# Performance work log

Hardware: AMD Instinct MI355X
Metric: run time of the kernel (lower is better)

The kernel has to match this reference:

```python
import jax, jax.numpy as jnp
import numpy as np

EPS = 1e-5

def _leaky(x):
    return jax.nn.leaky_relu(x, 0.2)

def _bn(x, p, axis):
    # p: [4, C] rows = (gamma, beta, running_mean, running_var); inference-mode BN
    g, b, m, v = p
    scale = g * jax.lax.rsqrt(v + EPS)
    shape = [1] * x.ndim
    shape[axis] = -1
    return x * scale.reshape(shape) + (b - m * scale).reshape(shape)

def _graph_feature(x, k):
    # x: [B, C, N] -> edge features [B, 2C, N, k] (knn on -squared-distance, topk largest)
    B, C, N = x.shape
    xx = jnp.sum(x * x, axis=1)                                   # [B, N]
    pd = 2.0 * jnp.einsum('bcn,bcm->bnm', x, x) - xx[:, :, None] - xx[:, None, :]
    idx = jax.lax.top_k(pd, k)[1]                                 # [B, N, k]
    xt = jnp.transpose(x, (0, 2, 1))                              # [B, N, C]
    nb = xt[jnp.arange(B)[:, None, None], idx]                    # [B, N, k, C]
    ctr = xt[:, :, None, :]
    f = jnp.concatenate([nb - ctr, jnp.broadcast_to(ctr, nb.shape)], axis=-1)
    return jnp.transpose(f, (0, 3, 1, 2))                         # [B, 2C, N, k]

def _cbam(x, fc1, fc2, sw):
    # Channel attention (shared MLP on avg+max pooled) then spatial attention (5x5 conv)
    mlp = lambda v: jax.nn.relu(v @ fc1.T) @ fc2.T
    ca = jax.nn.sigmoid(mlp(jnp.mean(x, (2, 3))) + mlp(jnp.max(x, (2, 3))))
    x = x * ca[:, :, None, None]
    s = jnp.concatenate([jnp.mean(x, 1, keepdims=True), jnp.max(x, 1, keepdims=True)], axis=1)
    sa = jax.lax.conv_general_dilated(s, sw, (1, 1), [(2, 2), (2, 2)],
                                      dimension_numbers=('NCHW', 'OIHW', 'NCHW'))
    return x * jax.nn.sigmoid(sa)

def _edge_block(x, k, W, bn, fc1, fc2, sw):
    f = _graph_feature(x, k)                                      # [B, 2C, N, k]
    f = _leaky(_bn(jnp.einsum('oc,bcnk->bonk', W, f), bn, 1))     # 1x1 conv + BN + LeakyReLU
    f = _cbam(f, fc1, fc2, sw)
    return jnp.max(f, axis=-1)                                    # [B, Cout, N]

def _bn_params(key, c):
    k1, k2, k3, k4 = jax.random.split(key, 4)
    g = 1.0 + 0.1 * jax.random.normal(k1, (c,))
    b = 0.1 * jax.random.normal(k2, (c,))
    m = 0.1 * jax.random.normal(k3, (c,))
    v = 0.5 + jax.random.uniform(k4, (c,))
    return jnp.stack([g, b, m, v])

def setup_inputs() -> dict:
    key = jax.random.key(0)
    nrm = lambda i, shape, s: s * jax.random.normal(jax.random.fold_in(key, i), shape, dtype=jnp.float32)
    d = {}
    d['x'] = jax.random.normal(jax.random.fold_in(key, 0), (4, 3, 2048), dtype=jnp.float32)
    d['W1'] = nrm(1, (64, 6), 0.3)
    d['W2'] = nrm(2, (64, 128), 0.15)
    d['W3'] = nrm(3, (128, 128), 0.15)
    d['W4'] = nrm(4, (256, 256), 0.1)
    d['W5'] = nrm(5, (1024, 512), 0.08)
    for i, c in zip(range(1, 6), [64, 64, 128, 256, 1024]):
        d['bn%d' % i] = _bn_params(jax.random.fold_in(key, 10 + i), c)
    d['bn6'] = _bn_params(jax.random.fold_in(key, 16), 512)
    d['bn7'] = _bn_params(jax.random.fold_in(key, 17), 256)
    for j, c in zip(range(1, 5), [64, 64, 128, 256]):
        r = c // 8
        d['ca%d_fc1' % j] = nrm(20 + j, (r, c), 0.2)
        d['ca%d_fc2' % j] = nrm(30 + j, (c, r), 0.2)
        d['sa%d' % j] = nrm(40 + j, (1, 2, 5, 5), 0.2)
    d['lin1_w'] = nrm(50, (512, 2048), 0.05)
    d['lin2_w'] = nrm(51, (256, 512), 0.08)
    d['lin2_b'] = nrm(52, (256,), 0.05)
    d['lin3_w'] = nrm(53, (40, 256), 0.1)
    d['lin3_b'] = nrm(54, (40,), 0.05)
    d['k'] = 20
    return d

def reference(x, W1, bn1, ca1_fc1, ca1_fc2, sa1, W2, bn2, ca2_fc1, ca2_fc2, sa2,
              W3, bn3, ca3_fc1, ca3_fc2, sa3, W4, bn4, ca4_fc1, ca4_fc2, sa4,
              W5, bn5, lin1_w, bn6, lin2_w, lin2_b, bn7, lin3_w, lin3_b, k):
    x1 = _edge_block(x,  k, W1, bn1, ca1_fc1, ca1_fc2, sa1)   # [B, 64, N]
    x2 = _edge_block(x1, k, W2, bn2, ca2_fc1, ca2_fc2, sa2)   # [B, 64, N]
    x3 = _edge_block(x2, k, W3, bn3, ca3_fc1, ca3_fc2, sa3)   # [B, 128, N]
    x4 = _edge_block(x3, k, W4, bn4, ca4_fc1, ca4_fc2, sa4)   # [B, 256, N]
    xc = jnp.concatenate([x1, x2, x3, x4], axis=1)            # [B, 512, N]
    h = _leaky(_bn(jnp.einsum('oc,bcn->bon', W5, xc), bn5, 1))  # [B, 1024, N]
    g = jnp.concatenate([jnp.max(h, axis=-1), jnp.mean(h, axis=-1)], axis=1)  # [B, 2048]
    g = _leaky(_bn(g @ lin1_w.T, bn6, 1))                     # dropout = identity (eval)
    g = _leaky(_bn(g @ lin2_w.T + lin2_b, bn7, 1))
    return g @ lin3_w.T + lin3_b                              # [B, 40]
```

## Files before the change

kernel.cpp:

```cpp
#include <hip/hip_runtime.h>
#include <math.h>

#define BB 4
#define NN 2048
#define KK 20
#define EPSF 1e-5f
#define TR 4

__device__ __forceinline__ float leaky(float x){ return x > 0.f ? x : 0.2f*x; }
__device__ __forceinline__ float sigm(float x){ return 1.f/(1.f+expf(-x)); }

__device__ __forceinline__ unsigned wave_umax_dpp(unsigned x){
  unsigned t;
  t = (unsigned)__builtin_amdgcn_update_dpp(0, (int)x, 0x111, 0xf, 0xf, true); x = x > t ? x : t;
  t = (unsigned)__builtin_amdgcn_update_dpp(0, (int)x, 0x112, 0xf, 0xf, true); x = x > t ? x : t;
  t = (unsigned)__builtin_amdgcn_update_dpp(0, (int)x, 0x114, 0xf, 0xf, true); x = x > t ? x : t;
  t = (unsigned)__builtin_amdgcn_update_dpp(0, (int)x, 0x118, 0xf, 0xf, true); x = x > t ? x : t;
  t = (unsigned)__builtin_amdgcn_update_dpp(0, (int)x, 0x142, 0xf, 0xf, true); x = x > t ? x : t;
  t = (unsigned)__builtin_amdgcn_update_dpp(0, (int)x, 0x143, 0xf, 0xf, true); x = x > t ? x : t;
  return (unsigned)__builtin_amdgcn_readlane((int)x, 63);
}

__global__ void k_xx(const float* __restrict__ X, long bstride, int C, float* __restrict__ xx){
  int i = blockIdx.x*blockDim.x + threadIdx.x;
  int b = i >> 11, n = i & (NN-1);
  const float* xb = X + (long)b*bstride;
  float s = 0.f;
  for (int c = 0; c < C; ++c){ float v = xb[c*NN + n]; s += v*v; }
  xx[i] = s;
}

__global__ __launch_bounds__(256) void k_knn(const float* __restrict__ X, long bstride, int C,
                      const float* __restrict__ xx, int* __restrict__ idx){
  __shared__ unsigned int pdrow[TR][NN];
  int rowsPerB = NN/TR;
  int b = blockIdx.x / rowsPerB;
  int r0 = (blockIdx.x % rowsPerB) * TR;
  const float* xb = X + (long)b*bstride;
  const float* xxb = xx + b*NN;
  int tid = threadIdx.x;
  int m0 = tid << 3;

  float acc[4][8];
  #pragma unroll
  for (int r = 0; r < 4; ++r)
    #pragma unroll
    for (int j = 0; j < 8; ++j) acc[r][j] = 0.f;
  for (int c = 0; c < C; ++c){
    const float* xcp = xb + (long)c*NN;
    float4 ctr = *(const float4*)(xcp + r0);
    float4 va = *(const float4*)(xcp + m0);
    float4 vb = *(const float4*)(xcp + m0 + 4);
    float v[8] = {va.x,va.y,va.z,va.w,vb.x,vb.y,vb.z,vb.w};
    #pragma unroll
    for (int j = 0; j < 8; ++j){
      acc[0][j] = fmaf(ctr.x, v[j], acc[0][j]);
      acc[1][j] = fmaf(ctr.y, v[j], acc[1][j]);
      acc[2][j] = fmaf(ctr.z, v[j], acc[2][j]);
      acc[3][j] = fmaf(ctr.w, v[j], acc[3][j]);
    }
  }
  float4 xr4 = *(const float4*)(xxb + r0);
  float xxr[4] = {xr4.x, xr4.y, xr4.z, xr4.w};
  float4 xma = *(const float4*)(xxb + m0);
  float4 xmb = *(const float4*)(xxb + m0 + 4);
  float xm[8] = {xma.x,xma.y,xma.z,xma.w,xmb.x,xmb.y,xmb.z,xmb.w};
  #pragma unroll
  for (int r = 0; r < 4; ++r){
    unsigned u[8];
    #pragma unroll
    for (int j = 0; j < 8; ++j){
      float pd = 2.f*acc[r][j] - xxr[r] - xm[j];
      unsigned uu = __float_as_uint(pd);
      uu ^= (uu & 0x80000000u) ? 0xFFFFFFFFu : 0x80000000u;
      u[j] = uu;
    }
    *(uint4*)&pdrow[r][m0]     = make_uint4(u[0],u[1],u[2],u[3]);
    *(uint4*)&pdrow[r][m0 + 4] = make_uint4(u[4],u[5],u[6],u[7]);
  }
  __syncthreads();

  int wave = tid >> 6, lane = tid & 63;
  int r = wave;
  unsigned long long k1 = 0ull, k2 = 0ull;
  #pragma unroll
  for (int j = 0; j < 32; ++j){
    int m = lane + (j<<6);
    unsigned long long key = ((unsigned long long)pdrow[r][m] << 11) | (unsigned)(2047 - m);
    if (key > k1){ k2 = k1; k1 = key; }
    else if (key > k2){ k2 = key; }
  }
  unsigned removed = 0u;
  int* orow = idx + ((long)b*NN + r0 + r)*KK;
  for (int sel = 0; sel < KK; ++sel){
    unsigned p = (unsigned)(k1 >> 11);
    unsigned g = wave_umax_dpp(p);
    unsigned long long tied = __ballot(p == g);
    if (__builtin_popcountll(tied) > 1){
      unsigned low = (p == g) ? (unsigned)(k1 & 2047ull) : 0u;
      unsigned gl = wave_umax_dpp(low);
      tied = __ballot((p == g) && (low == gl));
    }
    int owner = (int)__builtin_ctzll(tied);
    if (lane == owner){
      int gm = 2047 - (int)(k1 & 2047ull);
      orow[sel] = gm;
      removed |= 1u << (gm >> 6);
      k1 = k2; k2 = 0ull;
      if (k1 == 0ull && sel < KK-1){
        #pragma unroll
        for (int j = 0; j < 32; ++j){
          if (removed & (1u << j)) continue;
          int m = lane + (j<<6);
          unsigned long long key = ((unsigned long long)pdrow[r][m] << 11) | (unsigned)(2047 - m);
          if (key > k1){ k2 = k1; k1 = key; }
          else if (key > k2){ k2 = key; }
        }
      }
    }
  }
}

__global__ void k_proj(const float* __restrict__ X, long bstride, int C, int Cout,
                       const float* __restrict__ W, const float* __restrict__ bn,
                       float* __restrict__ Pg, float* __restrict__ PgT,
                       float* __restrict__ Pc, float* __restrict__ PcT){
  int nb = NN/256;
  int t = blockIdx.x;
  int nchunk = t % nb; t /= nb;
  int o = t % Cout; int b = t / Cout;
  int m = nchunk*256 + threadIdx.x;
  const float* xb = X + (long)b*bstride;
  float a1 = 0.f, a2 = 0.f;
  for (int c = 0; c < C; ++c){
    float v  = xb[c*NN + m];
    float wl = W[o*2*C + c], wr = W[o*2*C + C + c];
    a1 += wl*v; a2 += (wr - wl)*v;
  }
  float gg = bn[o], bb = bn[Cout+o], mn = bn[2*Cout+o], vv = bn[3*Cout+o];
  float scale = gg * rsqrtf(vv + EPSF);
  float bias  = bb - mn*scale;
  float pg = scale*a1;
  float pc = scale*a2 + bias;
  Pg [((long)b*Cout + o)*NN + m] = pg;
  PgT[((long)b*NN + m)*Cout + o] = pg;
  Pc [((long)b*Cout + o)*NN + m] = pc;
  PcT[((long)b*NN + m)*Cout + o] = pc;
}

__global__ __launch_bounds__(256) void k_proj_t(const float* __restrict__ X, long bstride, int C, int Cout,
                         const float* __restrict__ W, const float* __restrict__ bn,
                         float* __restrict__ Pg, float* __restrict__ PgT,
                         float* __restrict__ Pc, float* __restrict__ PcT){
  __shared__ float xs[32][128];
  __shared__ float wls[64][33];
  __shared__ float wds[64][33];
  int t = blockIdx.x;
  int nb = t & 15; t >>= 4;
  int nob = Cout >> 6;
  int ob = t % nob; int b = t / nob;
  int n0 = nb << 7, o0 = ob << 6;
  int tid = threadIdx.x;
  int tx = tid & 15, ty = tid >> 4;
  const float* xb = X + (long)b*bstride + n0;

  float ag[4][8], ac[4][8];
  #pragma unroll
  for (int i = 0; i < 4; ++i)
    #pragma unroll
    for (int j = 0; j < 8; ++j){ ag[i][j] = 0.f; ac[i][j] = 0.f; }

  for (int cc = 0; cc < C; cc += 32){
    {
      int col4 = tid & 31;
      int ci0 = tid >> 5;
      #pragma unroll
      for (int q = 0; q < 4; ++q){
        int ci = ci0 + (q << 3);
        float4 v = *(const float4*)(xb + (long)(cc + ci)*NN + (col4 << 2));
        *(float4*)&xs[ci][col4 << 2] = v;
      }
    }
    {
      int ci4 = tid & 7;
      int oi0 = tid >> 3;
      #pragma unroll
      for (int q = 0; q < 2; ++q){
        int oi = oi0 + (q << 5);
        const float* wrow = W + (long)(o0 + oi)*2*C + cc + (ci4 << 2);
        float4 wl = *(const float4*)(wrow);
        float4 wr = *(const float4*)(wrow + C);
        wls[oi][(ci4 << 2) + 0] = wl.x;
        wls[oi][(ci4 << 2) + 1] = wl.y;
        wls[oi][(ci4 << 2) + 2] = wl.z;
        wls[oi][(ci4 << 2) + 3] = wl.w;
        wds[oi][(ci4 << 2) + 0] = wr.x - wl.x;
        wds[oi][(ci4 << 2) + 1] = wr.y - wl.y;
        wds[oi][(ci4 << 2) + 2] = wr.z - wl.z;
        wds[oi][(ci4 << 2) + 3] = wr.w - wl.w;
      }
    }
    __syncthreads();
    #pragma unroll 8
    for (int ci = 0; ci < 32; ++ci){
      float4 xa  = *(const float4*)&xs[ci][tx << 2];
      float4 xc2 = *(const float4*)&xs[ci][64 + (tx << 2)];
      #pragma unroll
      for (int oo = 0; oo < 4; ++oo){
        float wl = wls[(ty << 2) + oo][ci];
        float wd = wds[(ty << 2) + oo][ci];
        ag[oo][0] = fmaf(wl, xa.x, ag[oo][0]); ag[oo][1] = fmaf(wl, xa.y, ag[oo][1]);
        ag[oo][2] = fmaf(wl, xa.z, ag[oo][2]); ag[oo][3] = fmaf(wl, xa.w, ag[oo][3]);
        ag[oo][4] = fmaf(wl, xc2.x, ag[oo][4]); ag[oo][5] = fmaf(wl, xc2.y, ag[oo][5]);
        ag[oo][6] = fmaf(wl, xc2.z, ag[oo][6]); ag[oo][7] = fmaf(wl, xc2.w, ag[oo][7]);
        ac[oo][0] = fmaf(wd, xa.x, ac[oo][0]); ac[oo][1] = fmaf(wd, xa.y, ac[oo][1]);
        ac[oo][2] = fmaf(wd, xa.z, ac[oo][2]); ac[oo][3] = fmaf(wd, xa.w, ac[oo][3]);
        ac[oo][4] = fmaf(wd, xc2.x, ac[oo][4]); ac[oo][5] = fmaf(wd, xc2.y, ac[oo][5]);
        ac[oo][6] = fmaf(wd, xc2.z, ac[oo][6]); ac[oo][7] = fmaf(wd, xc2.w, ac[oo][7]);
      }
    }
    __syncthreads();
  }

  float scl[4], bia[4];
  #pragma unroll
  for (int oo = 0; oo < 4; ++oo){
    int o = o0 + (ty << 2) + oo;
    scl[oo] = bn[o] * rsqrtf(bn[3*Cout + o] + EPSF);
    bia[oo] = bn[Cout + o] - bn[2*Cout + o]*scl[oo];
  }
  #pragma unroll
  for (int oo = 0; oo < 4; ++oo){
    long rb = ((long)b*Cout + o0 + (ty << 2) + oo)*NN + n0;
    float4 g0 = {scl[oo]*ag[oo][0], scl[oo]*ag[oo][1], scl[oo]*ag[oo][2], scl[oo]*ag[oo][3]};
    float4 g1 = {scl[oo]*ag[oo][4], scl[oo]*ag[oo][5], scl[oo]*ag[oo][6], scl[oo]*ag[oo][7]};
    float4 c0 = {fmaf(scl[oo], ac[oo][0], bia[oo]), fmaf(scl[oo], ac[oo][1], bia[oo]),
                 fmaf(scl[oo], ac[oo][2], bia[oo]), fmaf(scl[oo], ac[oo][3], bia[oo])};
    float4 c1 = {fmaf(scl[oo], ac[oo][4], bia[oo]), fmaf(scl[oo], ac[oo][5], bia[oo]),
                 fmaf(scl[oo], ac[oo][6], bia[oo]), fmaf(scl[oo], ac[oo][7], bia[oo])};
    *(float4*)(Pg + rb + (tx << 2))      = g0;
    *(float4*)(Pg + rb + 64 + (tx << 2)) = g1;
    *(float4*)(Pc + rb + (tx << 2))      = c0;
    *(float4*)(Pc + rb + 64 + (tx << 2)) = c1;
  }
  #pragma unroll
  for (int j = 0; j < 8; ++j){
    int n = n0 + ((j < 4) ? (tx << 2) + j : 64 + (tx << 2) + (j - 4));
    long rb = ((long)b*NN + n)*Cout + o0 + (ty << 2);
    float4 tg = {scl[0]*ag[0][j], scl[1]*ag[1][j], scl[2]*ag[2][j], scl[3]*ag[3][j]};
    float4 tc = {fmaf(scl[0], ac[0][j], bia[0]), fmaf(scl[1], ac[1][j], bia[1]),
                 fmaf(scl[2], ac[2][j], bia[2]), fmaf(scl[3], ac[3][j], bia[3])};
    *(float4*)(PgT + rb) = tg;
    *(float4*)(PcT + rb) = tc;
  }
}

__global__ void k_cstats(const float* __restrict__ Pg, const float* __restrict__ Pc,
                         const int* __restrict__ idx, int Cout,
                         float* __restrict__ cmean, float* __restrict__ cmax){
  int b = blockIdx.x / Cout, o = blockIdx.x % Cout;
  const float* pg = Pg + ((long)b*Cout + o)*NN;
  const float* pc = Pc + ((long)b*Cout + o)*NN;
  const int* id = idx + (long)b*NN*KK;
  int tid = threadIdx.x;
  float s = 0.f, mx = -INFINITY;
  for (int i = tid; i < NN*KK; i += 256){
    int n = i / KK;
    int iv = id[i];
    float v = leaky(pg[iv] + pc[n]);
    s += v; mx = fmaxf(mx, v);
  }
  __shared__ float ss[256], sm[256];
  ss[tid] = s; sm[tid] = mx; __syncthreads();
  for (int st = 128; st; st >>= 1){
    if (tid < st){ ss[tid] += ss[tid+st]; sm[tid] = fmaxf(sm[tid], sm[tid+st]); }
    __syncthreads();
  }
  if (tid == 0){ cmean[blockIdx.x] = ss[0]/(float)(NN*KK); cmax[blockIdx.x] = sm[0]; }
}

__global__ void k_catt(const float* __restrict__ cmean, const float* __restrict__ cmax,
                       const float* __restrict__ fc1, const float* __restrict__ fc2,
                       int Cout, int r, float* __restrict__ ca){
  int b = blockIdx.x, tid = threadIdx.x;
  __shared__ float h1m[32], h1x[32];
  __shared__ float mv[256], xv[256];
  if (tid < Cout){ mv[tid] = cmean[b*Cout+tid]; xv[tid] = cmax[b*Cout+tid]; }
  __syncthreads();
  if (tid < r){
    float am = 0.f, ax = 0.f;
    for (int c = 0; c < Cout; ++c){ float w = fc1[tid*Cout+c]; am += w*mv[c]; ax += w*xv[c]; }
    h1m[tid] = fmaxf(am, 0.f); h1x[tid] = fmaxf(ax, 0.f);
  }
  __syncthreads();
  if (tid < Cout){
    float a = 0.f;
    for (int j = 0; j < r; ++j) a += fc2[tid*r+j]*(h1m[j] + h1x[j]);
    ca[b*Cout+tid] = sigm(a);
  }
}

__global__ void k_sstats(const float* __restrict__ PgT, const float* __restrict__ PcT,
                         const int* __restrict__ idx, const float* __restrict__ ca,
                         int Cout, float* __restrict__ s){
  long i = (long)blockIdx.x*256 + threadIdx.x;
  int kk = (int)(i % KK); long t = i / KK; int n = (int)(t % NN); int b = (int)(t / NN);
  int iv = idx[((long)b*NN + n)*KK + kk];
  const float4* pg4 = (const float4*)(PgT + ((long)b*NN + iv)*Cout);
  const float4* pc4 = (const float4*)(PcT + ((long)b*NN + n)*Cout);
  const float4* ca4 = (const float4*)(ca + b*Cout);
  float sum = 0.f, mx = -INFINITY;
  int q = Cout >> 2;
  for (int o = 0; o < q; ++o){
    float4 a = pg4[o], c = pc4[o], w = ca4[o];
    float v0 = leaky(a.x + c.x) * w.x;
    float v1 = leaky(a.y + c.y) * w.y;
    float v2 = leaky(a.z + c.z) * w.z;
    float v3 = leaky(a.w + c.w) * w.w;
    sum += v0; mx = fmaxf(mx, v0);
    sum += v1; mx = fmaxf(mx, v1);
    sum += v2; mx = fmaxf(mx, v2);
    sum += v3; mx = fmaxf(mx, v3);
  }
  s[((long)b*2*NN + n)*KK + kk]      = sum/(float)Cout;
  s[((long)b*2*NN + NN + n)*KK + kk] = mx;
}

__global__ void k_sconv(const float* __restrict__ s, const float* __restrict__ sw,
                        float* __restrict__ sa){
  long i = (long)blockIdx.x*256 + threadIdx.x;
  int kk = (int)(i % KK); long t = i / KK; int n = (int)(t % NN); int b = (int)(t / NN);
  float acc = 0.f;
  for (int ci = 0; ci < 2; ++ci)
    for (int dy = 0; dy < 5; ++dy){
      int nn = n + dy - 2; if (nn < 0 || nn >= NN) continue;
      for (int dx = 0; dx < 5; ++dx){
        int kx = kk + dx - 2; if (kx < 0 || kx >= KK) continue;
        acc += sw[ci*25 + dy*5 + dx] * s[((long)b*2*NN + ci*NN + nn)*KK + kx];
      }
    }
  sa[i] = sigm(acc);
}

__global__ void k_final(const float* __restrict__ Pg, const float* __restrict__ Pc,
                        const int* __restrict__ idx, const float* __restrict__ ca,
                        const float* __restrict__ sa, int Cout, int outoff,
                        float* __restrict__ xc){
  long i = (long)blockIdx.x*256 + threadIdx.x;
  int n = (int)(i % NN); long t = i / NN; int o = (int)(t % Cout); int b = (int)(t / Cout);
  const float* pg = Pg + ((long)b*Cout + o)*NN;
  float pcv = Pc[((long)b*Cout + o)*NN + n];
  float cav = ca[b*Cout + o];
  const int* id   = idx + ((long)b*NN + n)*KK;
  const float* sb = sa  + ((long)b*NN + n)*KK;
  float mx = -INFINITY;
  for (int kk = 0; kk < KK; ++kk){
    float v = leaky(pg[id[kk]] + pcv) * cav * sb[kk];
    mx = fmaxf(mx, v);
  }
  xc[((long)b*512 + outoff + o)*NN + n] = mx;
}

__global__ __launch_bounds__(256) void k_gemm5(const float* __restrict__ xc, const float* __restrict__ W5,
                        const float* __restrict__ bn5, float* __restrict__ gpart){
  __shared__ float xs[32][128];
  __shared__ float wsd[64][33];
  int t = blockIdx.x;
  int nb = t & 15; t >>= 4;
  int ob = t & 15; int b = t >> 4;
  int n0 = nb << 7, o0 = ob << 6;
  int tid = threadIdx.x;
  int tx = tid & 15, ty = tid >> 4;
  const float* xb = xc + (long)b*512*NN + n0;

  float acc[4][8];
  #pragma unroll
  for (int i = 0; i < 4; ++i)
    #pragma unroll
    for (int j = 0; j < 8; ++j) acc[i][j] = 0.f;

  for (int cc = 0; cc < 16; ++cc){
    {
      int col4 = tid & 31;
      int ci0 = tid >> 5;
      #pragma unroll
      for (int q = 0; q < 4; ++q){
        int ci = ci0 + (q << 3);
        float4 v = *(const float4*)(xb + (long)(cc*32 + ci)*NN + (col4 << 2));
        *(float4*)&xs[ci][col4 << 2] = v;
      }
    }
    {
      int ci4 = tid & 7;
      int oi0 = tid >> 3;
      #pragma unroll
      for (int q = 0; q < 2; ++q){
        int oi = oi0 + (q << 5);
        float4 w = *(const float4*)(W5 + (long)(o0 + oi)*512 + cc*32 + (ci4 << 2));
        wsd[oi][(ci4 << 2) + 0] = w.x;
        wsd[oi][(ci4 << 2) + 1] = w.y;
        wsd[oi][(ci4 << 2) + 2] = w.z;
        wsd[oi][(ci4 << 2) + 3] = w.w;
      }
    }
    __syncthreads();
    #pragma unroll 8
    for (int ci = 0; ci < 32; ++ci){
      float4 xa = *(const float4*)&xs[ci][tx << 2];
      float4 xc2 = *(const float4*)&xs[ci][64 + (tx << 2)];
      float w0 = wsd[(ty << 2) + 0][ci];
      float w1 = wsd[(ty << 2) + 1][ci];
      float w2 = wsd[(ty << 2) + 2][ci];
      float w3 = wsd[(ty << 2) + 3][ci];
      acc[0][0] = fmaf(w0, xa.x, acc[0][0]); acc[0][1] = fmaf(w0, xa.y, acc[0][1]);
      acc[0][2] = fmaf(w0, xa.z, acc[0][2]); acc[0][3] = fmaf(w0, xa.w, acc[0][3]);
      acc[0][4] = fmaf(w0, xc2.x, acc[0][4]); acc[0][5] = fmaf(w0, xc2.y, acc[0][5]);
      acc[0][6] = fmaf(w0, xc2.z, acc[0][6]); acc[0][7] = fmaf(w0, xc2.w, acc[0][7]);
      acc[1][0] = fmaf(w1, xa.x, acc[1][0]); acc[1][1] = fmaf(w1, xa.y, acc[1][1]);
      acc[1][2] = fmaf(w1, xa.z, acc[1][2]); acc[1][3] = fmaf(w1, xa.w, acc[1][3]);
      acc[1][4] = fmaf(w1, xc2.x, acc[1][4]); acc[1][5] = fmaf(w1, xc2.y, acc[1][5]);
      acc[1][6] = fmaf(w1, xc2.z, acc[1][6]); acc[1][7] = fmaf(w1, xc2.w, acc[1][7]);
      acc[2][0] = fmaf(w2, xa.x, acc[2][0]); acc[2][1] = fmaf(w2, xa.y, acc[2][1]);
      acc[2][2] = fmaf(w2, xa.z, acc[2][2]); acc[2][3] = fmaf(w2, xa.w, acc[2][3]);
      acc[2][4] = fmaf(w2, xc2.x, acc[2][4]); acc[2][5] = fmaf(w2, xc2.y, acc[2][5]);
      acc[2][6] = fmaf(w2, xc2.z, acc[2][6]); acc[2][7] = fmaf(w2, xc2.w, acc[2][7]);
      acc[3][0] = fmaf(w3, xa.x, acc[3][0]); acc[3][1] = fmaf(w3, xa.y, acc[3][1]);
      acc[3][2] = fmaf(w3, xa.z, acc[3][2]); acc[3][3] = fmaf(w3, xa.w, acc[3][3]);
      acc[3][4] = fmaf(w3, xc2.x, acc[3][4]); acc[3][5] = fmaf(w3, xc2.y, acc[3][5]);
      acc[3][6] = fmaf(w3, xc2.z, acc[3][6]); acc[3][7] = fmaf(w3, xc2.w, acc[3][7]);
    }
    __syncthreads();
  }

  float psum[4], pmax[4];
  #pragma unroll
  for (int oo = 0; oo < 4; ++oo){
    int o = o0 + (ty << 2) + oo;
    float scale = bn5[o] * rsqrtf(bn5[3072 + o] + EPSF);
    float bias  = bn5[1024 + o] - bn5[2048 + o] * scale;
    float s = 0.f, mx = -INFINITY;
    #pragma unroll
    for (int j = 0; j < 8; ++j){
      float v = leaky(fmaf(scale, acc[oo][j], bias));
      s += v; mx = fmaxf(mx, v);
    }
    psum[oo] = s; pmax[oo] = mx;
  }
  __syncthreads();
  float* ps = &xs[0][0];
  float* pm = ps + 64*17;
  #pragma unroll
  for (int oo = 0; oo < 4; ++oo){
    int o = (ty << 2) + oo;
    ps[o*17 + tx] = psum[oo];
    pm[o*17 + tx] = pmax[oo];
  }
  __syncthreads();
  if (tid < 64){
    float s = 0.f, mx = -INFINITY;
    #pragma unroll
    for (int j = 0; j < 16; ++j){
      s += ps[tid*17 + j];
      mx = fmaxf(mx, pm[tid*17 + j]);
    }
    long base = ((long)(b*16 + nb))*1024 + o0 + tid;
    gpart[base] = s;
    gpart[65536 + base] = mx;
  }
}

__global__ void k_pool2(const float* __restrict__ gpart, float* __restrict__ g){
  int i = blockIdx.x*256 + threadIdx.x;
  int b = i >> 10, o = i & 1023;
  float s = 0.f, mx = -INFINITY;
  for (int nb = 0; nb < 16; ++nb){
    s += gpart[((long)(b*16 + nb))*1024 + o];
    mx = fmaxf(mx, gpart[65536 + ((long)(b*16 + nb))*1024 + o]);
  }
  g[b*2048 + o] = mx;
  g[b*2048 + 1024 + o] = s * (1.f/2048.f);
}

__global__ void k_dense(const float* __restrict__ in, const float* __restrict__ w,
                        const float* __restrict__ bias, const float* __restrict__ bnp,
                        int Cin, int Cout, float* __restrict__ out){
  int b = blockIdx.x / Cout, j = blockIdx.x % Cout;
  int tid = threadIdx.x;
  float a = 0.f;
  for (int c = tid; c < Cin; c += 256) a += w[(long)j*Cin + c]*in[(long)b*Cin + c];
  __shared__ float ss[256];
  ss[tid] = a; __syncthreads();
  for (int st = 128; st; st >>= 1){
    if (tid < st) ss[tid] += ss[tid+st];
    __syncthreads();
  }
  if (tid == 0){
    float v = ss[0];
    if (bias) v += bias[j];
    if (bnp){
      float scale = bnp[j]*rsqrtf(bnp[3*Cout+j] + EPSF);
      float bb    = bnp[Cout+j] - bnp[2*Cout+j]*scale;
      v = leaky(v*scale + bb);
    }
    out[b*Cout + j] = v;
  }
}

extern "C" void kernel_launch(void* const* d_in, const int* in_sizes, int n_in,
                              void* d_out, int out_size, void* d_ws, size_t ws_size,
                              hipStream_t stream){
  (void)in_sizes; (void)n_in; (void)out_size;
  const float* x  = (const float*)d_in[0];
  const float* Wb[4]  = {(const float*)d_in[1], (const float*)d_in[2], (const float*)d_in[3], (const float*)d_in[4]};
  const float* W5     = (const float*)d_in[5];
  const float* bnb[4] = {(const float*)d_in[6], (const float*)d_in[7], (const float*)d_in[8], (const float*)d_in[9]};
  const float* bn5    = (const float*)d_in[10];
  const float* bn6    = (const float*)d_in[11];
  const float* bn7    = (const float*)d_in[12];
  const float* fc1b[4] = {(const float*)d_in[13], (const float*)d_in[16], (const float*)d_in[19], (const float*)d_in[22]};
  const float* fc2b[4] = {(const float*)d_in[14], (const float*)d_in[17], (const float*)d_in[20], (const float*)d_in[23]};
  const float* swb[4]  = {(const float*)d_in[15], (const float*)d_in[18], (const float*)d_in[21], (const float*)d_in[24]};
  const float* lin1_w = (const float*)d_in[25];
  const float* lin2_w = (const float*)d_in[26];
  const float* lin2_b = (const float*)d_in[27];
  const float* lin3_w = (const float*)d_in[28];
  const float* lin3_b = (const float*)d_in[29];

  float* ws = (float*)d_ws;
  float* xc = ws;
  float* tb = ws + (size_t)BB*512*NN;
  float* xx   = tb;
  int*   idx  = (int*)(tb + 8192);
  float* Pg   = tb + 8192 + 163840;
  float* PgT  = Pg  + 2097152;
  float* Pc   = PgT + 2097152;
  float* PcT  = Pc  + 2097152;
  float* cmean = PcT + 2097152;
  float* cmax  = cmean + 1024;
  float* ca    = cmax + 1024;
  float* s     = ca + 1024;
  float* sa    = s + 327680;
  float* gpart = tb;
  float* g  = tb + 131072;
  float* t1 = g + 8192;
  float* t2 = t1 + 2048;
  size_t needed = ((size_t)BB*512*NN + 9055232) * 4;
  if (ws_size < needed) return;

  const int Cin [4] = {3, 64, 64, 128};
  const int Cout[4] = {64, 64, 128, 256};
  const int inoff[4]  = {0, 0, 64, 128};
  const int outoff[4] = {0, 64, 128, 256};

  for (int blk = 0; blk < 4; ++blk){
    const float* Xp; long bstr;
    if (blk == 0){ Xp = x; bstr = 3l*NN; }
    else { Xp = xc + (long)inoff[blk]*NN; bstr = 512l*NN; }
    int C = Cin[blk], Co = Cout[blk];
    hipLaunchKernelGGL(k_xx,    dim3(BB*NN/256), dim3(256), 0, stream, Xp, bstr, C, xx);
    hipLaunchKernelGGL(k_knn,   dim3(BB*NN/TR),  dim3(256), 0, stream, Xp, bstr, C, xx, idx);
    if (blk == 0){
      hipLaunchKernelGGL(k_proj,  dim3(BB*Co*(NN/256)), dim3(256), 0, stream, Xp, bstr, C, Co, Wb[blk], bnb[blk], Pg, PgT, Pc, PcT);
    } else {
      hipLaunchKernelGGL(k_proj_t, dim3(BB*(Co>>6)*16), dim3(256), 0, stream, Xp, bstr, C, Co, Wb[blk], bnb[blk], Pg, PgT, Pc, PcT);
    }
    hipLaunchKernelGGL(k_cstats, dim3(BB*Co), dim3(256), 0, stream, Pg, Pc, idx, Co, cmean, cmax);
    hipLaunchKernelGGL(k_catt,  dim3(BB), dim3(256), 0, stream, cmean, cmax, fc1b[blk], fc2b[blk], Co, Co/8, ca);
    hipLaunchKernelGGL(k_sstats, dim3(BB*NN*KK/256), dim3(256), 0, stream, PgT, PcT, idx, ca, Co, s);
    hipLaunchKernelGGL(k_sconv, dim3(BB*NN*KK/256), dim3(256), 0, stream, s, swb[blk], sa);
    hipLaunchKernelGGL(k_final, dim3(BB*Co*NN/256), dim3(256), 0, stream, Pg, Pc, idx, ca, sa, Co, outoff[blk], xc);
  }
  hipLaunchKernelGGL(k_gemm5, dim3(BB*16*16), dim3(256), 0, stream, xc, W5, bn5, gpart);
  hipLaunchKernelGGL(k_pool2, dim3(16), dim3(256), 0, stream, gpart, g);
  hipLaunchKernelGGL(k_dense, dim3(BB*512), dim3(256), 0, stream, g,  lin1_w, (const float*)nullptr, bn6, 2048, 512, t1);
  hipLaunchKernelGGL(k_dense, dim3(BB*256), dim3(256), 0, stream, t1, lin2_w, lin2_b, bn7, 512, 256, t2);
  hipLaunchKernelGGL(k_dense, dim3(BB*40),  dim3(256), 0, stream, t2, lin3_w, lin3_b, (const float*)nullptr, 256, 40, (float*)d_out);
}
```

Measured before the change: 1.066 ms.

## Chunk kNN distance rows with per-lane top-4 lists and transpose GEMM5 weight tile

The kNN kernel now computes pairwise distances in two 1024-column chunks and keeps a top-4 sorted list per lane instead of top-2. This halves the shared-memory distance buffer and sets a 6-blocks-per-SM launch bound to raise occupancy. When a lane's list runs out during selection, it recomputes distances from global memory rather than rereading shared memory, which can be costly if it happens often. Separately, the GEMM5 weight tile is stored transposed so each thread reads four weights with one float4 shared load.

Result: slower. 1.996 ms (+87.3%).

```diff
diff --git a/kernel.cpp b/kernel.cpp
--- a/kernel.cpp
+++ b/kernel.cpp
@@ -21,6 +21,12 @@
   return (unsigned)__builtin_amdgcn_readlane((int)x, 63);
 }
 
+__device__ __forceinline__ void ce64(unsigned long long &a, unsigned long long &b){
+  unsigned long long mx = a > b ? a : b;
+  unsigned long long mn = a > b ? b : a;
+  a = mx; b = mn;
+}
+
 __global__ void k_xx(const float* __restrict__ X, long bstride, int C, float* __restrict__ xx){
   int i = blockIdx.x*blockDim.x + threadIdx.x;
   int b = i >> 11, n = i & (NN-1);
@@ -30,91 +36,99 @@
   xx[i] = s;
 }
 
-__global__ __launch_bounds__(256) void k_knn(const float* __restrict__ X, long bstride, int C,
+__global__ __launch_bounds__(256, 6) void k_knn(const float* __restrict__ X, long bstride, int C,
                       const float* __restrict__ xx, int* __restrict__ idx){
-  __shared__ unsigned int pdrow[TR][NN];
+  __shared__ unsigned int pdc[TR][1024];
   int rowsPerB = NN/TR;
   int b = blockIdx.x / rowsPerB;
   int r0 = (blockIdx.x % rowsPerB) * TR;
   const float* xb = X + (long)b*bstride;
   const float* xxb = xx + b*NN;
   int tid = threadIdx.x;
-  int m0 = tid << 3;
-
-  float acc[4][8];
-  #pragma unroll
-  for (int r = 0; r < 4; ++r)
-    #pragma unroll
-    for (int j = 0; j < 8; ++j) acc[r][j] = 0.f;
-  for (int c = 0; c < C; ++c){
-    const float* xcp = xb + (long)c*NN;
-    float4 ctr = *(const float4*)(xcp + r0);
-    float4 va = *(const float4*)(xcp + m0);
-    float4 vb = *(const float4*)(xcp + m0 + 4);
-    float v[8] = {va.x,va.y,va.z,va.w,vb.x,vb.y,vb.z,vb.w};
-    #pragma unroll
-    for (int j = 0; j < 8; ++j){
-      acc[0][j] = fmaf(ctr.x, v[j], acc[0][j]);
-      acc[1][j] = fmaf(ctr.y, v[j], acc[1][j]);
-      acc[2][j] = fmaf(ctr.z, v[j], acc[2][j]);
-      acc[3][j] = fmaf(ctr.w, v[j], acc[3][j]);
-    }
-  }
+  int lane = tid & 63, wave = tid >> 6;
+
   float4 xr4 = *(const float4*)(xxb + r0);
   float xxr[4] = {xr4.x, xr4.y, xr4.z, xr4.w};
-  float4 xma = *(const float4*)(xxb + m0);
-  float4 xmb = *(const float4*)(xxb + m0 + 4);
-  float xm[8] = {xma.x,xma.y,xma.z,xma.w,xmb.x,xmb.y,xmb.z,xmb.w};
-  #pragma unroll
-  for (int r = 0; r < 4; ++r){
-    unsigned u[8];
-    #pragma unroll
-    for (int j = 0; j < 8; ++j){
-      float pd = 2.f*acc[r][j] - xxr[r] - xm[j];
-      unsigned uu = __float_as_uint(pd);
-      uu ^= (uu & 0x80000000u) ? 0xFFFFFFFFu : 0x80000000u;
-      u[j] = uu;
-    }
-    *(uint4*)&pdrow[r][m0]     = make_uint4(u[0],u[1],u[2],u[3]);
-    *(uint4*)&pdrow[r][m0 + 4] = make_uint4(u[4],u[5],u[6],u[7]);
-  }
-  __syncthreads();
-
-  int wave = tid >> 6, lane = tid & 63;
-  int r = wave;
-  unsigned long long k1 = 0ull, k2 = 0ull;
-  #pragma unroll
-  for (int j = 0; j < 32; ++j){
-    int m = lane + (j<<6);
-    unsigned long long key = ((unsigned long long)pdrow[r][m] << 11) | (unsigned)(2047 - m);
-    if (key > k1){ k2 = k1; k1 = key; }
-    else if (key > k2){ k2 = key; }
-  }
+
+  unsigned long long s0 = 0ull, s1 = 0ull, s2 = 0ull, s3 = 0ull;
+
+  for (int ch = 0; ch < 2; ++ch){
+    int mb = ch << 10;
+    int m0 = mb + (tid << 2);
+    float acc[4][4];
+    #pragma unroll
+    for (int r = 0; r < 4; ++r){ acc[r][0]=0.f; acc[r][1]=0.f; acc[r][2]=0.f; acc[r][3]=0.f; }
+    for (int c = 0; c < C; ++c){
+      const float* xcp = xb + (long)c*NN;
+      float4 ctr = *(const float4*)(xcp + r0);
+      float4 v   = *(const float4*)(xcp + m0);
+      float cr[4] = {ctr.x, ctr.y, ctr.z, ctr.w};
+      #pragma unroll
+      for (int r = 0; r < 4; ++r){
+        acc[r][0] = fmaf(cr[r], v.x, acc[r][0]);
+        acc[r][1] = fmaf(cr[r], v.y, acc[r][1]);
+        acc[r][2] = fmaf(cr[r], v.z, acc[r][2]);
+        acc[r][3] = fmaf(cr[r], v.w, acc[r][3]);
+      }
+    }
+    float4 xmv = *(const float4*)(xxb + m0);
+    float xm[4] = {xmv.x, xmv.y, xmv.z, xmv.w};
+    #pragma unroll
+    for (int r = 0; r < 4; ++r){
+      unsigned u[4];
+      #pragma unroll
+      for (int q = 0; q < 4; ++q){
+        float pd = 2.f*acc[r][q] - xxr[r] - xm[q];
+        unsigned uu = __float_as_uint(pd);
+        uu ^= (uu & 0x80000000u) ? 0xFFFFFFFFu : 0x80000000u;
+        u[q] = uu;
+      }
+      *(uint4*)&pdc[r][tid << 2] = make_uint4(u[0],u[1],u[2],u[3]);
+    }
+    __syncthreads();
+    #pragma unroll
+    for (int jj = 0; jj < 16; ++jj){
+      int mloc = lane + (jj << 6);
+      int m = mb + mloc;
+      unsigned long long key = ((unsigned long long)pdc[wave][mloc] << 11) | (unsigned)(2047 - m);
+      s3 = s3 > key ? s3 : key;
+      ce64(s2, s3); ce64(s1, s2); ce64(s0, s1);
+    }
+    __syncthreads();
+  }
+
+  int rowg = r0 + wave;
+  int* orow = idx + ((long)b*NN + rowg)*KK;
+  float xxrow = xxr[wave];
   unsigned removed = 0u;
-  int* orow = idx + ((long)b*NN + r0 + r)*KK;
   for (int sel = 0; sel < KK; ++sel){
-    unsigned p = (unsigned)(k1 >> 11);
+    unsigned p = (unsigned)(s0 >> 11);
     unsigned g = wave_umax_dpp(p);
     unsigned long long tied = __ballot(p == g);
     if (__builtin_popcountll(tied) > 1){
-      unsigned low = (p == g) ? (unsigned)(k1 & 2047ull) : 0u;
+      unsigned low = (p == g) ? (unsigned)(s0 & 2047ull) : 0u;
       unsigned gl = wave_umax_dpp(low);
       tied = __ballot((p == g) && (low == gl));
     }
     int owner = (int)__builtin_ctzll(tied);
     if (lane == owner){
-      int gm = 2047 - (int)(k1 & 2047ull);
+      int gm = 2047 - (int)(s0 & 2047ull);
       orow[sel] = gm;
       removed |= 1u << (gm >> 6);
-      k1 = k2; k2 = 0ull;
-      if (k1 == 0ull && sel < KK-1){
-        #pragma unroll
+      s0 = s1; s1 = s2; s2 = s3; s3 = 0ull;
+      if (s0 == 0ull && sel < KK-1){
         for (int j = 0; j < 32; ++j){
-          if (removed & (1u << j)) continue;
-          int m = lane + (j<<6);
-          unsigned long long key = ((unsigned long long)pdrow[r][m] << 11) | (unsigned)(2047 - m);
-          if (key > k1){ k2 = k1; k1 = key; }
-          else if (key > k2){ k2 = key; }
+          if ((removed >> j) & 1u) continue;
+          int m = lane + (j << 6);
+          float d = 0.f;
+          for (int c = 0; c < C; ++c)
+            d = fmaf(xb[(long)c*NN + rowg], xb[(long)c*NN + m], d);
+          float pd = 2.f*d - xxrow - xxb[m];
+          unsigned uu = __float_as_uint(pd);
+          uu ^= (uu & 0x80000000u) ? 0xFFFFFFFFu : 0x80000000u;
+          unsigned long long key = ((unsigned long long)uu << 11) | (unsigned)(2047 - m);
+          s3 = s3 > key ? s3 : key;
+          ce64(s2, s3); ce64(s1, s2); ce64(s0, s1);
         }
       }
     }
@@ -364,7 +378,7 @@
 __global__ __launch_bounds__(256) void k_gemm5(const float* __restrict__ xc, const float* __restrict__ W5,
                         const float* __restrict__ bn5, float* __restrict__ gpart){
   __shared__ float xs[32][128];
-  __shared__ float wsd[64][33];
+  __shared__ float wst[32][68];
   int t = blockIdx.x;
   int nb = t & 15; t >>= 4;
   int ob = t & 15; int b = t >> 4;
@@ -397,10 +411,10 @@
       for (int q = 0; q < 2; ++q){
         int oi = oi0 + (q << 5);
         float4 w = *(const float4*)(W5 + (long)(o0 + oi)*512 + cc*32 + (ci4 << 2));
-        wsd[oi][(ci4 << 2) + 0] = w.x;
-        wsd[oi][(ci4 << 2) + 1] = w.y;
-        wsd[oi][(ci4 << 2) + 2] = w.z;
-        wsd[oi][(ci4 << 2) + 3] = w.w;
+        wst[(ci4 << 2) + 0][oi] = w.x;
+        wst[(ci4 << 2) + 1][oi] = w.y;
+        wst[(ci4 << 2) + 2][oi] = w.z;
+        wst[(ci4 << 2) + 3][oi] = w.w;
       }
     }
     __syncthreads();
@@ -408,10 +422,8 @@
     for (int ci = 0; ci < 32; ++ci){
       float4 xa = *(const float4*)&xs[ci][tx << 2];
       float4 xc2 = *(const float4*)&xs[ci][64 + (tx << 2)];
-      float w0 = wsd[(ty << 2) + 0][ci];
-      float w1 = wsd[(ty << 2) + 1][ci];
-      float w2 = wsd[(ty << 2) + 2][ci];
-      float w3 = wsd[(ty << 2) + 3][ci];
+      float4 wv = *(const float4*)&wst[ci][ty << 2];
+      float w0 = wv.x, w1 = wv.y, w2 = wv.z, w3 = wv.w;
       acc[0][0] = fmaf(w0, xa.x, acc[0][0]); acc[0][1] = fmaf(w0, xa.y, acc[0][1]);
       acc[0][2] = fmaf(w0, xa.z, acc[0][2]); acc[0][3] = fmaf(w0, xa.w, acc[0][3]);
       acc[0][4] = fmaf(w0, xc2.x, acc[0][4]); acc[0][5] = fmaf(w0, xc2.y, acc[0][5]);
```

## Split kNN into tiled pairwise-distance GEMM and separate top-k selection kernel

Applied to the files above, without the earlier changes.

The fused kNN kernel computed four rows of the distance matrix per block by streaming every feature column from global memory, so the X reads were not reused across rows. It is replaced by a shared-memory-tiled GEMM kernel (64x128 tiles, 32-channel chunks) that writes full distance rows to workspace memory aliased over the projection buffers. A separate selection kernel then reads each row back with vectorised loads and runs the same wave-level top-k. Both are issued twice, for two batches at a time, so the rows fit in the reused workspace. The cost is an extra global write and read of a 2x2048x2048 matrix per half-batch and more kernel launches.

Result: slower. 1.165 ms (+9.3%).

```diff
diff --git a/kernel.cpp b/kernel.cpp
--- a/kernel.cpp
+++ b/kernel.cpp
@@ -5,7 +5,6 @@
 #define NN 2048
 #define KK 20
 #define EPSF 1e-5f
-#define TR 4
 
 __device__ __forceinline__ float leaky(float x){ return x > 0.f ? x : 0.2f*x; }
 __device__ __forceinline__ float sigm(float x){ return 1.f/(1.f+expf(-x)); }
@@ -30,68 +29,114 @@
   xx[i] = s;
 }
 
-__global__ __launch_bounds__(256) void k_knn(const float* __restrict__ X, long bstride, int C,
-                      const float* __restrict__ xx, int* __restrict__ idx){
-  __shared__ unsigned int pdrow[TR][NN];
-  int rowsPerB = NN/TR;
-  int b = blockIdx.x / rowsPerB;
-  int r0 = (blockIdx.x % rowsPerB) * TR;
+__global__ __launch_bounds__(256) void k_pd(const float* __restrict__ X, long bstride, int C,
+                     const float* __restrict__ xx, int bbase, unsigned* __restrict__ pd2){
+  __shared__ float xn[32][64];
+  __shared__ float xm[32][128];
+  int t = blockIdx.x;
+  int mb = t & 15; t >>= 4;
+  int nb = t & 31; t >>= 5;
+  int b2 = t;
+  int b = bbase + b2;
+  int n0 = nb << 6, m0 = mb << 7;
   const float* xb = X + (long)b*bstride;
   const float* xxb = xx + b*NN;
   int tid = threadIdx.x;
-  int m0 = tid << 3;
+  int tx = tid & 15, ty = tid >> 4;
 
   float acc[4][8];
   #pragma unroll
-  for (int r = 0; r < 4; ++r)
+  for (int i = 0; i < 4; ++i)
     #pragma unroll
-    for (int j = 0; j < 8; ++j) acc[r][j] = 0.f;
-  for (int c = 0; c < C; ++c){
-    const float* xcp = xb + (long)c*NN;
-    float4 ctr = *(const float4*)(xcp + r0);
-    float4 va = *(const float4*)(xcp + m0);
-    float4 vb = *(const float4*)(xcp + m0 + 4);
-    float v[8] = {va.x,va.y,va.z,va.w,vb.x,vb.y,vb.z,vb.w};
-    #pragma unroll
-    for (int j = 0; j < 8; ++j){
-      acc[0][j] = fmaf(ctr.x, v[j], acc[0][j]);
-      acc[1][j] = fmaf(ctr.y, v[j], acc[1][j]);
-      acc[2][j] = fmaf(ctr.z, v[j], acc[2][j]);
-      acc[3][j] = fmaf(ctr.w, v[j], acc[3][j]);
-    }
-  }
-  float4 xr4 = *(const float4*)(xxb + r0);
-  float xxr[4] = {xr4.x, xr4.y, xr4.z, xr4.w};
-  float4 xma = *(const float4*)(xxb + m0);
-  float4 xmb = *(const float4*)(xxb + m0 + 4);
-  float xm[8] = {xma.x,xma.y,xma.z,xma.w,xmb.x,xmb.y,xmb.z,xmb.w};
-  #pragma unroll
-  for (int r = 0; r < 4; ++r){
+    for (int j = 0; j < 8; ++j) acc[i][j] = 0.f;
+
+  for (int cc = 0; cc < C; cc += 32){
+    {
+      int col4 = tid & 15;
+      int ci0 = tid >> 4;
+      #pragma unroll
+      for (int q = 0; q < 2; ++q){
+        int ci = ci0 + (q << 4);
+        float4 v = make_float4(0.f,0.f,0.f,0.f);
+        if (cc + ci < C) v = *(const float4*)(xb + (long)(cc + ci)*NN + n0 + (col4 << 2));
+        *(float4*)&xn[ci][col4 << 2] = v;
+      }
+    }
+    {
+      int col4 = tid & 31;
+      int ci0 = tid >> 5;
+      #pragma unroll
+      for (int q = 0; q < 4; ++q){
+        int ci = ci0 + (q << 3);
+        float4 v = make_float4(0.f,0.f,0.f,0.f);
+        if (cc + ci < C) v = *(const float4*)(xb + (long)(cc + ci)*NN + m0 + (col4 << 2));
+        *(float4*)&xm[ci][col4 << 2] = v;
+      }
+    }
+    __syncthreads();
+    #pragma unroll 8
+    for (int ci = 0; ci < 32; ++ci){
+      float4 ma = *(const float4*)&xm[ci][tx << 2];
+      float4 mb2 = *(const float4*)&xm[ci][64 + (tx << 2)];
+      #pragma unroll
+      for (int oo = 0; oo < 4; ++oo){
+        float w = xn[ci][(ty << 2) + oo];
+        acc[oo][0] = fmaf(w, ma.x, acc[oo][0]); acc[oo][1] = fmaf(w, ma.y, acc[oo][1]);
+        acc[oo][2] = fmaf(w, ma.z, acc[oo][2]); acc[oo][3] = fmaf(w, ma.w, acc[oo][3]);
+        acc[oo][4] = fmaf(w, mb2.x, acc[oo][4]); acc[oo][5] = fmaf(w, mb2.y, acc[oo][5]);
+        acc[oo][6] = fmaf(w, mb2.z, acc[oo][6]); acc[oo][7] = fmaf(w, mb2.w, acc[oo][7]);
+      }
+    }
+    __syncthreads();
+  }
+
+  float4 xma = *(const float4*)(xxb + m0 + (tx << 2));
+  float4 xmb = *(const float4*)(xxb + m0 + 64 + (tx << 2));
+  float xm8[8] = {xma.x,xma.y,xma.z,xma.w,xmb.x,xmb.y,xmb.z,xmb.w};
+  #pragma unroll
+  for (int oo = 0; oo < 4; ++oo){
+    int n = n0 + (ty << 2) + oo;
+    float xxn = xxb[n];
     unsigned u[8];
     #pragma unroll
     for (int j = 0; j < 8; ++j){
-      float pd = 2.f*acc[r][j] - xxr[r] - xm[j];
+      float pd = 2.f*acc[oo][j] - xxn - xm8[j];
       unsigned uu = __float_as_uint(pd);
       uu ^= (uu & 0x80000000u) ? 0xFFFFFFFFu : 0x80000000u;
       u[j] = uu;
     }
-    *(uint4*)&pdrow[r][m0]     = make_uint4(u[0],u[1],u[2],u[3]);
-    *(uint4*)&pdrow[r][m0 + 4] = make_uint4(u[4],u[5],u[6],u[7]);
-  }
-  __syncthreads();
-
-  int wave = tid >> 6, lane = tid & 63;
-  int r = wave;
+    unsigned* prow = pd2 + ((long)b2*NN + n)*NN + m0;
+    *(uint4*)(prow + (tx << 2))      = make_uint4(u[0],u[1],u[2],u[3]);
+    *(uint4*)(prow + 64 + (tx << 2)) = make_uint4(u[4],u[5],u[6],u[7]);
+  }
+}
+
+__global__ __launch_bounds__(256) void k_sel(const unsigned* __restrict__ pd2, int bbase,
+                      int* __restrict__ idx){
+  int t = blockIdx.x;
+  int b2 = t >> 9;
+  int r0 = (t & 511) << 2;
+  int tid = threadIdx.x;
+  int lane = tid & 63, wave = tid >> 6;
+  int row = r0 + wave;
+  const unsigned* prow = pd2 + ((long)b2*NN + row)*NN;
+
   unsigned long long k1 = 0ull, k2 = 0ull;
   #pragma unroll
-  for (int j = 0; j < 32; ++j){
-    int m = lane + (j<<6);
-    unsigned long long key = ((unsigned long long)pdrow[r][m] << 11) | (unsigned)(2047 - m);
-    if (key > k1){ k2 = k1; k1 = key; }
-    else if (key > k2){ k2 = key; }
+  for (int j = 0; j < 8; ++j){
+    int m = (lane << 2) + (j << 8);
+    uint4 u = *(const uint4*)(prow + m);
+    unsigned uv[4] = {u.x, u.y, u.z, u.w};
+    #pragma unroll
+    for (int q = 0; q < 4; ++q){
+      unsigned long long key = ((unsigned long long)uv[q] << 11) | (unsigned)(2047 - (m + q));
+      if (key > k1){ k2 = k1; k1 = key; }
+      else if (key > k2){ k2 = key; }
+    }
   }
   unsigned removed = 0u;
-  int* orow = idx + ((long)b*NN + r0 + r)*KK;
+  int b = bbase + b2;
+  int* orow = idx + ((long)b*NN + row)*KK;
   for (int sel = 0; sel < KK; ++sel){
     unsigned p = (unsigned)(k1 >> 11);
     unsigned g = wave_umax_dpp(p);
@@ -105,16 +150,21 @@
     if (lane == owner){
       int gm = 2047 - (int)(k1 & 2047ull);
       orow[sel] = gm;
-      removed |= 1u << (gm >> 6);
+      removed |= 1u << (((gm >> 8) << 2) | (gm & 3));
       k1 = k2; k2 = 0ull;
       if (k1 == 0ull && sel < KK-1){
         #pragma unroll
-        for (int j = 0; j < 32; ++j){
-          if (removed & (1u << j)) continue;
-          int m = lane + (j<<6);
-          unsigned long long key = ((unsigned long long)pdrow[r][m] << 11) | (unsigned)(2047 - m);
-          if (key > k1){ k2 = k1; k1 = key; }
-          else if (key > k2){ k2 = key; }
+        for (int j = 0; j < 8; ++j){
+          int m = (lane << 2) + (j << 8);
+          uint4 u = *(const uint4*)(prow + m);
+          unsigned uv[4] = {u.x, u.y, u.z, u.w};
+          #pragma unroll
+          for (int q = 0; q < 4; ++q){
+            if (removed & (1u << ((j << 2) | q))) continue;
+            unsigned long long key = ((unsigned long long)uv[q] << 11) | (unsigned)(2047 - (m + q));
+            if (key > k1){ k2 = k1; k1 = key; }
+            else if (key > k2){ k2 = key; }
+          }
         }
       }
     }
@@ -540,6 +590,7 @@
   float* ca    = cmax + 1024;
   float* s     = ca + 1024;
   float* sa    = s + 327680;
+  unsigned* pd2 = (unsigned*)Pg;
   float* gpart = tb;
   float* g  = tb + 131072;
   float* t1 = g + 8192;
@@ -557,8 +608,11 @@
     if (blk == 0){ Xp = x; bstr = 3l*NN; }
     else { Xp = xc + (long)inoff[blk]*NN; bstr = 512l*NN; }
     int C = Cin[blk], Co = Cout[blk];
-    hipLaunchKernelGGL(k_xx,    dim3(BB*NN/256), dim3(256), 0, stream, Xp, bstr, C, xx);
-    hipLaunchKernelGGL(k_knn,   dim3(BB*NN/TR),  dim3(256), 0, stream, Xp, bstr, C, xx, idx);
+    hipLaunchKernelGGL(k_xx,  dim3(BB*NN/256), dim3(256), 0, stream, Xp, bstr, C, xx);
+    hipLaunchKernelGGL(k_pd,  dim3(2*32*16), dim3(256), 0, stream, Xp, bstr, C, xx, 0, pd2);
+    hipLaunchKernelGGL(k_sel, dim3(2*NN/4),  dim3(256), 0, stream, pd2, 0, idx);
+    hipLaunchKernelGGL(k_pd,  dim3(2*32*16), dim3(256), 0, stream, Xp, bstr, C, xx, 2, pd2);
+    hipLaunchKernelGGL(k_sel, dim3(2*NN/4),  dim3(256), 0, stream, pd2, 2, idx);
     if (blk == 0){
       hipLaunchKernelGGL(k_proj,  dim3(BB*Co*(NN/256)), dim3(256), 0, stream, Xp, bstr, C, Co, Wb[blk], bnb[blk], Pg, PgT, Pc, PcT);
     } else {
```
